# Kernel optimization log

Hardware: AMD Instinct MI355X
Metric: run time of the kernel (lower is better)

## Reference

```python
import jax, jax.numpy as jnp
import numpy as np

D, K, N = 20, 256, 8192


def setup_inputs() -> dict:
    key = jax.random.key(0)
    k1, k2, k3 = jax.random.split(key, 3)
    # sparse count observations -> dense float32 counts
    obs = jax.random.randint(k1, (N, K), 0, 5).astype(jnp.float32)
    beta0 = jax.random.uniform(k2, (1, K), dtype=jnp.float32)
    beta1 = jax.random.uniform(k3, (K, K, D), dtype=jnp.float32)
    return {"obs": obs, "beta0": beta0, "beta1": beta1, "tau": D, "t": N}


def reference(obs, beta0, beta1, tau, t):
    """Equivalent of TorchNetPoissonProcess.forward(tau, t).

    The per-step sparse kron eta construction + mm(eta, beta.T) collapses to:
      lam_{t'}[k] = beta0[k] + sum_{a,k'} beta1[k,k',a] * obs[t'-d+a, k']
    Vectorized over all t' in [tau, t) via sliding windows.
    """
    d = beta1.shape[2]
    T = t - tau  # number of timesteps (static Python int)
    wins = jnp.stack(
        [jax.lax.dynamic_slice_in_dim(obs, tau - d + a, T, axis=0) for a in range(d)],
        axis=1,
    )
    lam = beta0 + jnp.einsum('tab,kba->tk', wins, beta1)
    obs_t = jax.lax.dynamic_slice_in_dim(obs, tau, T, axis=0)  # [T, K]
    # sum_t [ <obs_t, log lam_t> - sum_k lam_t[k] ]
    loglik = jnp.sum(obs_t * jnp.log(lam)) - jnp.sum(lam)
    return loglik, lam
```

## Files before the change

### kernel.cpp

```cpp
#include <hip/hip_runtime.h>

#define KDIM 256
#define DWIN 20
#define NOBS 8192
#define TAU  20
#define TROWS (NOBS - TAU)
#define KTOT  (DWIN * KDIM)
#define KS128 (KTOT / 128)
#define QS128 (KS128 / 4)

#define BM 64
#define NBLK_M ((TROWS + BM - 1) / BM)
#define NBLK   (NBLK_M * 4)

#define AROWS 83
#define APITCH 272

#define PC_BYTES  65536
#define SRED_OFF  PC_BYTES
#define DYN_TOTAL (PC_BYTES + 64)

typedef float f32x4 __attribute__((ext_vector_type(4)));
typedef int   i32x4 __attribute__((ext_vector_type(4)));
typedef int   i32x8 __attribute__((ext_vector_type(8)));

#define WS_BF    0u
#define WS_NEED  (1310720u + 8192u)

__device__ __forceinline__ i32x8 join8(i32x4 a, i32x4 b) {
    i32x8 r;
    r[0]=a[0]; r[1]=a[1]; r[2]=a[2]; r[3]=a[3];
    r[4]=b[0]; r[5]=b[1]; r[6]=b[2]; r[7]=b[3];
    return r;
}

__device__ __forceinline__ unsigned int pk4_fp8(float a, float b, float c, float d) {
    int lo = __builtin_amdgcn_cvt_pk_fp8_f32(a, b, 0, false);
    return (unsigned int)__builtin_amdgcn_cvt_pk_fp8_f32(c, d, lo, true);
}

__global__ __launch_bounds__(256)
void prep_bfrag_kernel(const float* __restrict__ beta1,
                       unsigned char* __restrict__ Bf8,
                       float* __restrict__ out)
{
    __shared__ float L[KDIM * 21];
    const int n   = blockIdx.x;
    const int tid = threadIdx.x;
    if (n == 0 && tid == 0) out[0] = 0.f;

    const float* __restrict__ src = beta1 + (size_t)n * KTOT;
    for (int f = tid; f < KTOT; f += 256)
        L[(f / DWIN) * 21 + (f % DWIN)] = src[f];
    __syncthreads();

    const int nt = n >> 4, qn = n & 15;
    for (int c = tid; c < KS128 * 8; c += 256) {
        const int ks = c >> 3, g = (c >> 1) & 3, half = c & 1;
        const int kb = ks * 128 + g * 32 + half * 16;
        i32x4 w;
#pragma unroll
        for (int u = 0; u < 4; ++u) {
            const int k0 = kb + u * 4;
            w[u] = (int)pk4_fp8(L[((k0+0) & 255) * 21 + ((k0+0) >> 8)],
                                L[((k0+1) & 255) * 21 + ((k0+1) >> 8)],
                                L[((k0+2) & 255) * 21 + ((k0+2) >> 8)],
                                L[((k0+3) & 255) * 21 + ((k0+3) >> 8)]);
        }
        *(i32x4*)&Bf8[(((size_t)ks * 16 + nt) * 64 + g * 16 + qn) * 32 + half * 16] = w;
    }
}

extern __shared__ char dynlds[];

__global__ __launch_bounds__(256, 2)
void gemm_kernel(const float* __restrict__ obs,
                 const float* __restrict__ beta0,
                 const unsigned char* __restrict__ Bf8,
                 float* __restrict__ out)
{
    const int tid  = threadIdx.x;
    const int lane = tid & 63;
    const int kq   = tid >> 6;
    const int g = lane >> 4;
    const int q = lane & 15;
    const int nb = blockIdx.x & 3;
    const int mb = blockIdx.x >> 2;
    const int i0 = mb * BM;

    char* ldsA8 = dynlds;

    const char* bbase = (const char*)Bf8 + (size_t)(nb * 4) * 2048 + (size_t)lane * 32;

#define LOADB8(dst, s)                                                           \
    {                                                                            \
        const char* _p = bbase + (size_t)(10 * kq + ((s) < QS128 ? (s) : QS128 - 1)) * 32768; \
        _Pragma("unroll")                                                        \
        for (int t = 0; t < 4; ++t) {                                            \
            i32x4 _lo = *(const i32x4*)(_p + t * 2048);                          \
            i32x4 _hi = *(const i32x4*)(_p + t * 2048 + 16);                     \
            dst[t] = join8(_lo, _hi);                                            \
        }                                                                        \
    }

    i32x8 rbA[4], rbB[4];
    LOADB8(rbA, 0)

    for (int idx = tid; idx < AROWS * 64; idx += 256) {
        int row = idx >> 6, c4 = idx & 63;
        int grow = min(i0 + row, NOBS - 1);
        float4 v = ((const float4*)obs)[(size_t)grow * 64 + c4];
        *(unsigned int*)(ldsA8 + row * APITCH + c4 * 4) = pk4_fp8(v.x, v.y, v.z, v.w);
    }
    __syncthreads();

    f32x4 acc[4][4];
#pragma unroll
    for (int m = 0; m < 4; ++m)
#pragma unroll
        for (int t = 0; t < 4; ++t)
            acc[m][t] = (f32x4){0.f, 0.f, 0.f, 0.f};

#define COMPUTE8(s, breg)                                                        \
    {                                                                            \
        const int _ks = 10 * kq + (s);                                           \
        const int _aro  = _ks >> 1;                                              \
        const int _acol = (_ks & 1) * 128 + g * 32;                              \
        i32x8 _af[4];                                                            \
        _Pragma("unroll")                                                        \
        for (int m = 0; m < 4; ++m) {                                            \
            const char* _ap = ldsA8 + (m * 16 + q + _aro) * APITCH + _acol;      \
            i32x4 _lo = *(const i32x4*)_ap;                                      \
            i32x4 _hi = *(const i32x4*)(_ap + 16);                               \
            _af[m] = join8(_lo, _hi);                                            \
        }                                                                        \
        _Pragma("unroll")                                                        \
        for (int t = 0; t < 4; ++t)                                              \
            _Pragma("unroll")                                                    \
            for (int m = 0; m < 4; ++m)                                          \
                acc[m][t] = __builtin_amdgcn_mfma_scale_f32_16x16x128_f8f6f4(    \
                    _af[m], (breg)[t], acc[m][t], 0, 0, 0, 0x7f, 0, 0x7f);       \
    }

#pragma unroll 1
    for (int s = 0; s < QS128; s += 2) {
        LOADB8(rbB, s + 1)
        COMPUTE8(s, rbA)
        if (s + 2 < QS128) LOADB8(rbA, s + 2)
        COMPUTE8(s + 1, rbB)
    }

    __syncthreads();
    f32x4* pc = (f32x4*)dynlds;
#pragma unroll
    for (int m = 0; m < 4; ++m)
#pragma unroll
        for (int t = 0; t < 4; ++t)
            pc[((kq * 16 + m * 4 + t) << 6) + lane] = acc[m][t];
    __syncthreads();

    double part = 0.0;
#pragma unroll
    for (int t = 0; t < 4; ++t) {
        f32x4 sum = pc[((kq * 4 + t) << 6) + lane];
#pragma unroll
        for (int wp = 1; wp < 4; ++wp)
            sum += pc[((wp * 16 + kq * 4 + t) << 6) + lane];
        const int col = nb * 64 + t * 16 + q;
        const float b0v = beta0[col];
#pragma unroll
        for (int r = 0; r < 4; ++r) {
            const int row = i0 + kq * 16 + 4 * g + r;
            if (row < TROWS) {
                float lam = sum[r] + b0v;
                out[1 + (size_t)row * KDIM + col] = lam;
                float o = obs[(size_t)(row + TAU) * KDIM + col];
                part += (double)o * (double)__logf(lam) - (double)lam;
            }
        }
    }

#pragma unroll
    for (int off = 32; off > 0; off >>= 1) part += __shfl_down(part, off, 64);
    double* sred = (double*)(dynlds + SRED_OFF);
    if (lane == 0) sred[kq] = part;
    __syncthreads();
    if (tid == 0)
        atomicAdd(out, (float)(sred[0] + sred[1] + sred[2] + sred[3]));
}

#define BM_OLD 16
#define NBLK_OLD ((TROWS + BM_OLD - 1) / BM_OLD)

__global__ __launch_bounds__(KDIM, 2)
void old_lam_kernel(const float* __restrict__ obs,
                    const float* __restrict__ beta0,
                    const float* __restrict__ beta1,
                    float* __restrict__ out,
                    double* __restrict__ partials)
{
    const int k  = threadIdx.x;
    const int i0 = blockIdx.x * BM_OLD;
    const int nr = min(BM_OLD, TROWS - i0);
    const int smax = nr + DWIN - 1;

    float acc[BM_OLD];
#pragma unroll
    for (int r = 0; r < BM_OLD; ++r) acc[r] = 0.f;

    const float* __restrict__ b1k = beta1 + (size_t)k * (KDIM * DWIN);

    for (int b = 0; b < KDIM; ++b) {
        float br[DWIN];
        const float4* qd = (const float4*)(b1k + b * DWIN);
#pragma unroll
        for (int v = 0; v < DWIN / 4; ++v) {
            float4 t = qd[v];
            br[4*v+0] = t.x; br[4*v+1] = t.y; br[4*v+2] = t.z; br[4*v+3] = t.w;
        }
        float wv[BM_OLD + DWIN - 1];
#pragma unroll
        for (int s = 0; s < BM_OLD + DWIN - 1; ++s)
            wv[s] = (s < smax) ? obs[(size_t)(i0 + s) * KDIM + b] : 0.f;
#pragma unroll
        for (int r = 0; r < BM_OLD; ++r)
#pragma unroll
            for (int a = 0; a < DWIN; ++a)
                acc[r] = fmaf(wv[r + a], br[a], acc[r]);
    }

    const float b0 = beta0[k];
    double part = 0.0;
    for (int r = 0; r < nr; ++r) {
        float lam = acc[r] + b0;
        out[1 + (size_t)(i0 + r) * KDIM + k] = lam;
        float o = obs[(size_t)(i0 + r + TAU) * KDIM + k];
        part += (double)(o * logf(lam) - lam);
    }

    __shared__ double sred2[KDIM];
    sred2[k] = part;
    __syncthreads();
    for (int off = KDIM / 2; off > 0; off >>= 1) {
        if (k < off) sred2[k] += sred2[k + off];
        __syncthreads();
    }
    if (k == 0) partials[blockIdx.x] = sred2[0];
}

__global__ void reduce_final_kernel(const double* __restrict__ partials,
                                    float* __restrict__ out, int n)
{
    __shared__ double sr[256];
    double v = 0.0;
    for (int i = threadIdx.x; i < n; i += 256) v += partials[i];
    sr[threadIdx.x] = v;
    __syncthreads();
    for (int off = 128; off > 0; off >>= 1) {
        if (threadIdx.x < off) sr[threadIdx.x] += sr[threadIdx.x + off];
        __syncthreads();
    }
    if (threadIdx.x == 0) out[0] = (float)sr[0];
}

extern "C" void kernel_launch(void* const* d_in, const int* in_sizes, int n_in,
                              void* d_out, int out_size, void* d_ws, size_t ws_size,
                              hipStream_t stream)
{
    const float* obs   = (const float*)d_in[0];
    const float* beta0 = (const float*)d_in[1];
    const float* beta1 = (const float*)d_in[2];
    float* out = (float*)d_out;

    if (ws_size >= (size_t)WS_NEED) {
        unsigned char* Bf8 = (unsigned char*)d_ws + WS_BF;

        (void)hipFuncSetAttribute(reinterpret_cast<const void*>(gemm_kernel),
                                  hipFuncAttributeMaxDynamicSharedMemorySize,
                                  DYN_TOTAL);

        hipLaunchKernelGGL(prep_bfrag_kernel, dim3(KDIM), dim3(256), 0, stream,
                           beta1, Bf8, out);
        hipLaunchKernelGGL(gemm_kernel, dim3(NBLK), dim3(256), DYN_TOTAL, stream,
                           obs, beta0, Bf8, out);
    } else {
        double* partials = (double*)d_ws;
        hipLaunchKernelGGL(old_lam_kernel, dim3(NBLK_OLD), dim3(KDIM), 0, stream,
                           obs, beta0, beta1, out, partials);
        hipLaunchKernelGGL(reduce_final_kernel, dim3(1), dim3(256), 0, stream,
                           partials, out, NBLK_OLD);
    }
}
```

Before: 35.27 us.

## Pre-convert obs to fp8 in prep kernel and stream A fragments from global

The obs matrix is converted to fp8 once in the prep kernel, which gets 64 extra blocks for this, instead of each gemm block converting its window into LDS. The gemm kernel then loads A fragments straight from global memory into registers, double-buffered alongside the B fragments, which removes the LDS staging and the barrier before the main loop. The cost is a larger workspace, one extra pass writing 2 MB of fp8 data, and more register pressure from the extra A buffers. A-tile reuse now relies on the L2 cache rather than LDS.

```diff
diff --git a/kernel.cpp b/kernel.cpp
--- a/kernel.cpp
+++ b/kernel.cpp
@@ -13,9 +13,6 @@
 #define NBLK_M ((TROWS + BM - 1) / BM)
 #define NBLK   (NBLK_M * 4)
 
-#define AROWS 83
-#define APITCH 272
-
 #define PC_BYTES  65536
 #define SRED_OFF  PC_BYTES
 #define DYN_TOTAL (PC_BYTES + 64)
@@ -25,7 +22,8 @@
 typedef int   i32x8 __attribute__((ext_vector_type(8)));
 
 #define WS_BF    0u
-#define WS_NEED  (1310720u + 8192u)
+#define WS_A8    2097152u
+#define WS_NEED  (WS_A8 + 2097152u + 8192u)
 
 __device__ __forceinline__ i32x8 join8(i32x4 a, i32x4 b) {
     i32x8 r;
@@ -40,13 +38,25 @@
 }
 
 __global__ __launch_bounds__(256)
-void prep_bfrag_kernel(const float* __restrict__ beta1,
-                       unsigned char* __restrict__ Bf8,
-                       float* __restrict__ out)
-{
+void prep_kernel(const float* __restrict__ beta1,
+                 const float* __restrict__ obs,
+                 unsigned char* __restrict__ Bf8,
+                 unsigned int* __restrict__ A8,
+                 float* __restrict__ out)
+{
+    const int tid = threadIdx.x;
+    if (blockIdx.x >= KDIM) {
+        const int base = (blockIdx.x - KDIM) * 8192;
+#pragma unroll 4
+        for (int u = tid; u < 8192; u += 256) {
+            float4 v = ((const float4*)obs)[base + u];
+            A8[base + u] = pk4_fp8(v.x, v.y, v.z, v.w);
+        }
+        return;
+    }
+
     __shared__ float L[KDIM * 21];
-    const int n   = blockIdx.x;
-    const int tid = threadIdx.x;
+    const int n = blockIdx.x;
     if (n == 0 && tid == 0) out[0] = 0.f;
 
     const float* __restrict__ src = beta1 + (size_t)n * KTOT;
@@ -77,6 +87,7 @@
 void gemm_kernel(const float* __restrict__ obs,
                  const float* __restrict__ beta0,
                  const unsigned char* __restrict__ Bf8,
+                 const unsigned char* __restrict__ A8,
                  float* __restrict__ out)
 {
     const int tid  = threadIdx.x;
@@ -87,8 +98,6 @@
     const int nb = blockIdx.x & 3;
     const int mb = blockIdx.x >> 2;
     const int i0 = mb * BM;
-
-    char* ldsA8 = dynlds;
 
     const char* bbase = (const char*)Bf8 + (size_t)(nb * 4) * 2048 + (size_t)lane * 32;
 
@@ -103,16 +112,24 @@
         }                                                                        \
     }
 
-    i32x8 rbA[4], rbB[4];
+#define LOADA8(dst, s)                                                           \
+    {                                                                            \
+        const int _ks = 10 * kq + ((s) < QS128 ? (s) : QS128 - 1);               \
+        const int _aro  = _ks >> 1;                                              \
+        const int _acol = (_ks & 1) * 128 + g * 32;                              \
+        _Pragma("unroll")                                                        \
+        for (int m = 0; m < 4; ++m) {                                            \
+            const int _row = min(i0 + m * 16 + q + _aro, NOBS - 1);              \
+            const char* _ap = (const char*)A8 + (size_t)_row * 256 + _acol;      \
+            i32x4 _lo = *(const i32x4*)_ap;                                      \
+            i32x4 _hi = *(const i32x4*)(_ap + 16);                               \
+            dst[m] = join8(_lo, _hi);                                            \
+        }                                                                        \
+    }
+
+    i32x8 raA[4], raB[4], rbA[4], rbB[4];
+    LOADA8(raA, 0)
     LOADB8(rbA, 0)
-
-    for (int idx = tid; idx < AROWS * 64; idx += 256) {
-        int row = idx >> 6, c4 = idx & 63;
-        int grow = min(i0 + row, NOBS - 1);
-        float4 v = ((const float4*)obs)[(size_t)grow * 64 + c4];
-        *(unsigned int*)(ldsA8 + row * APITCH + c4 * 4) = pk4_fp8(v.x, v.y, v.z, v.w);
-    }
-    __syncthreads();
 
     f32x4 acc[4][4];
 #pragma unroll
@@ -121,36 +138,28 @@
         for (int t = 0; t < 4; ++t)
             acc[m][t] = (f32x4){0.f, 0.f, 0.f, 0.f};
 
-#define COMPUTE8(s, breg)                                                        \
+#define COMPUTE8(areg, breg)                                                     \
     {                                                                            \
-        const int _ks = 10 * kq + (s);                                           \
-        const int _aro  = _ks >> 1;                                              \
-        const int _acol = (_ks & 1) * 128 + g * 32;                              \
-        i32x8 _af[4];                                                            \
-        _Pragma("unroll")                                                        \
-        for (int m = 0; m < 4; ++m) {                                            \
-            const char* _ap = ldsA8 + (m * 16 + q + _aro) * APITCH + _acol;      \
-            i32x4 _lo = *(const i32x4*)_ap;                                      \
-            i32x4 _hi = *(const i32x4*)(_ap + 16);                               \
-            _af[m] = join8(_lo, _hi);                                            \
-        }                                                                        \
         _Pragma("unroll")                                                        \
         for (int t = 0; t < 4; ++t)                                              \
             _Pragma("unroll")                                                    \
             for (int m = 0; m < 4; ++m)                                          \
                 acc[m][t] = __builtin_amdgcn_mfma_scale_f32_16x16x128_f8f6f4(    \
-                    _af[m], (breg)[t], acc[m][t], 0, 0, 0, 0x7f, 0, 0x7f);       \
+                    (areg)[m], (breg)[t], acc[m][t], 0, 0, 0, 0x7f, 0, 0x7f);    \
     }
 
 #pragma unroll 1
     for (int s = 0; s < QS128; s += 2) {
+        LOADA8(raB, s + 1)
         LOADB8(rbB, s + 1)
-        COMPUTE8(s, rbA)
-        if (s + 2 < QS128) LOADB8(rbA, s + 2)
-        COMPUTE8(s + 1, rbB)
-    }
-
-    __syncthreads();
+        COMPUTE8(raA, rbA)
+        if (s + 2 < QS128) {
+            LOADA8(raA, s + 2)
+            LOADB8(rbA, s + 2)
+        }
+        COMPUTE8(raB, rbB)
+    }
+
     f32x4* pc = (f32x4*)dynlds;
 #pragma unroll
     for (int m = 0; m < 4; ++m)
@@ -274,15 +283,16 @@
 
     if (ws_size >= (size_t)WS_NEED) {
         unsigned char* Bf8 = (unsigned char*)d_ws + WS_BF;
+        unsigned int*  A8  = (unsigned int*)((char*)d_ws + WS_A8);
 
         (void)hipFuncSetAttribute(reinterpret_cast<const void*>(gemm_kernel),
                                   hipFuncAttributeMaxDynamicSharedMemorySize,
                                   DYN_TOTAL);
 
-        hipLaunchKernelGGL(prep_bfrag_kernel, dim3(KDIM), dim3(256), 0, stream,
-                           beta1, Bf8, out);
+        hipLaunchKernelGGL(prep_kernel, dim3(KDIM + 64), dim3(256), 0, stream,
+                           beta1, obs, Bf8, A8, out);
         hipLaunchKernelGGL(gemm_kernel, dim3(NBLK), dim3(256), DYN_TOTAL, stream,
-                           obs, beta0, Bf8, out);
+                           obs, beta0, Bf8, (const unsigned char*)A8, out);
     } else {
         double* partials = (double*)d_ws;
         hipLaunchKernelGGL(old_lam_kernel, dim3(NBLK_OLD), dim3(KDIM), 0, stream,
```

Result: slower. 51.74 us (+46.7%).
